# Performance work log

Measured on AMD Instinct MI355X. Metric: run time of the kernel, lower is better.

## Reference

```python
import jax, jax.numpy as jnp
import numpy as np

B, T, U, K, CDIM, S, M = 128, 600, 96, 10, 80, 512, 20
D1 = 3 + CDIM        # rnn1 input: x_t (3) + attention window w (CDIM)
D2 = 3 + S + CDIM    # rnn2 / rnn3 input: x_t + prev rnn out + w
OUT_DIM = 1 + 6 * M


def setup_inputs() -> dict:
    key = jax.random.key(0)
    ks = jax.random.split(key, 16)
    g = lambda k, shape: jax.random.normal(k, shape, jnp.float32) * 0.05
    z = lambda n: jnp.zeros((n,), jnp.float32)
    return {
        "x": jax.random.normal(ks[0], (B, T, 3), jnp.float32),
        "c_vec": jax.random.uniform(ks[1], (B, U, CDIM), jnp.float32),
        # FF cell 1 (input dim D1)
        "W_jx1": g(ks[2], (D1, S)), "b_jx1": z(S),
        "W_jh1": g(ks[3], (S, S)),  "b_jh1": z(S),
        "W_kx1": g(ks[4], (D1, S)), "b_kx1": z(S),
        "W_kh1": g(ks[5], (S, S)),  "b_kh1": z(S),
        # FF cell 2 (input dim D2) -- also used for the 3rd RNN (source reuses self.rnn2)
        "W_jx2": g(ks[6], (D2, S)), "b_jx2": z(S),
        "W_jh2": g(ks[7], (S, S)),  "b_jh2": z(S),
        "W_kx2": g(ks[8], (D2, S)), "b_kx2": z(S),
        "W_kh2": g(ks[9], (S, S)),  "b_kh2": z(S),
        # attention window head: S -> 3K
        "W_win": g(ks[10], (S, 3 * K)), "b_win": z(3 * K),
        # output head: S -> 1 + 6M
        "W_lin": g(ks[11], (S, OUT_DIM)), "b_lin": z(OUT_DIM),
    }


def _ff(inp, h, Wjx, bjx, Wjh, bjh, Wkx, bkx, Wkh, bkh):
    # custom gated cell: out = j*(1-h) + (1-k)*h
    j = jax.nn.sigmoid(inp @ Wjx + bjx + h @ Wjh + bjh)
    k = jax.nn.sigmoid(inp @ Wkx + bkx + h @ Wkh + bkh)
    return j * (1.0 - h) + (1.0 - k) * h


def reference(x, c_vec,
              W_jx1, b_jx1, W_jh1, b_jh1, W_kx1, b_kx1, W_kh1, b_kh1,
              W_jx2, b_jx2, W_jh2, b_jh2, W_kx2, b_kx2, W_kh2, b_kh2,
              W_win, b_win, W_lin, b_lin):
    u = jnp.arange(U, dtype=x.dtype)  # [U]

    def step(carry, xt):
        h1, h2, h3, kappa, w = carry  # h*: [B,S], kappa: [B,K], w: [B,CDIM]
        in1 = jnp.concatenate([xt, w], axis=-1)
        h1 = _ff(in1, h1, W_jx1, b_jx1, W_jh1, b_jh1, W_kx1, b_kx1, W_kh1, b_kh1)
        kg = h1 @ W_win + b_win                       # [B, 3K]
        a_hat, be_hat, k_hat = jnp.split(kg, 3, axis=1)
        alpha = jnp.exp(a_hat)                        # [B,K]
        beta = jnp.exp(be_hat)
        kappa = kappa + jnp.exp(k_hat)
        # phi[b,u] = sum_k alpha * exp(-beta * (kappa - u)^2)
        phi = jnp.sum(alpha[:, :, None] *
                      jnp.exp(-beta[:, :, None] * (kappa[:, :, None] - u) ** 2),
                      axis=1)                          # [B,U]
        w = jnp.einsum('bu,buc->bc', phi, c_vec)      # [B,CDIM]
        in2 = jnp.concatenate([xt, h1, w], axis=-1)
        h2 = _ff(in2, h2, W_jx2, b_jx2, W_jh2, b_jh2, W_kx2, b_kx2, W_kh2, b_kh2)
        in3 = jnp.concatenate([xt, h2, w], axis=-1)
        # source bug kept faithfully: third RNN reuses rnn2's weights
        h3 = _ff(in3, h3, W_jx2, b_jx2, W_jh2, b_jh2, W_kx2, b_kx2, W_kh2, b_kh2)
        return (h1, h2, h3, kappa, w), h3

    zS = jnp.zeros((B, S), x.dtype)
    init = (zS, zS, zS, jnp.zeros((B, K), x.dtype), jnp.zeros((B, CDIM), x.dtype))
    _, ys = jax.lax.scan(step, init, jnp.swapaxes(x, 0, 1))  # ys: [T,B,S]
    out_cat = jnp.swapaxes(ys, 0, 1).reshape(B * T, S)
    return out_cat @ W_lin + b_lin                    # [B*T, 1+6M]
```

## Files before the change

### kernel.cpp

```cpp
#include <hip/hip_runtime.h>
#include <hip/hip_bf16.h>

typedef __bf16 bf16;
typedef __bf16 bf16x8 __attribute__((ext_vector_type(8)));
typedef float  f32x4  __attribute__((ext_vector_type(4)));

#define AS1 __attribute__((address_space(1)))
#define AS3 __attribute__((address_space(3)))

#define NT   600
#define NB   128
#define NS   512
#define NU   96
#define NK   10
#define NC   80
#define NOUT 121

#define W1X_J 0
#define W1W_J 16384
#define W1H_J 65536
#define W1X_K 327680
#define W1W_K 344064
#define W1H_K 393216
#define W2X_J 655360
#define W2W_J 671744
#define W2A_J 720896
#define W2H_J 983040
#define W2X_K 1245184
#define W2W_K 1261568
#define W2A_K 1310720
#define W2H_K 1572864
#define WWIN  1835008
#define WLIN  1851392

#define BIAS_BYTE_OFF 3833856
#define H_BYTE_OFF    3842048
#define HBUF 65536
#define FLAG_BYTE_OFF 4659200
#define BAR_BYTE_OFF  4659264

#define HSTRIDE 520

#define AUX_SC0   1
#define AUX_SC0S1 17

__device__ __forceinline__ float ldIn(const void* q, long i, int isF32) {
  if (isF32) return ((const float*)q)[i];
  return (float)((const bf16*)q)[i];
}

struct KParams {
  const void* x;
  const void* c_vec;
  const void* b_win;
  const void* b_lin;
  const bf16* W;
  const float* bias;
  bf16* h1; bf16* h2; bf16* h3;
  void* out;
  const int* flag;
  int* bar;
};

template <int AUX>
__device__ __forceinline__ void stage_tile_async(const bf16* g, bf16* lds, int tid) {
  const int w = tid >> 6, lane = tid & 63;
#pragma unroll
  for (int r = 0; r < 4; ++r) {
    const int row = (w << 2) + r;
    __builtin_amdgcn_global_load_lds(
        (const AS1 void*)(g + (size_t)row * NS + (size_t)lane * 8),
        (AS3 void*)(lds + (size_t)row * HSTRIDE), 16, 0, AUX);
  }
}

__device__ __forceinline__ void group_arrive(int* gb) {
  __syncthreads();
  if (threadIdx.x == 0) {
    if ((__hip_atomic_fetch_add(gb, 1, __ATOMIC_RELAXED, __HIP_MEMORY_SCOPE_AGENT) & 31) == 31)
      __hip_atomic_fetch_add(gb + 8, 1, __ATOMIC_RELAXED, __HIP_MEMORY_SCOPE_AGENT);
  }
}
__device__ __forceinline__ void group_wait(int* gb, int target) {
  if (threadIdx.x == 0) {
    while (__hip_atomic_load(gb + 8, __ATOMIC_RELAXED, __HIP_MEMORY_SCOPE_AGENT) < target)
      __builtin_amdgcn_s_sleep(1);
  }
  __syncthreads();
  __atomic_signal_fence(__ATOMIC_ACQ_REL);
}

__device__ __forceinline__ void storeH(unsigned* dst, unsigned v, bool fast) {
  if (fast) *dst = v;
  else __hip_atomic_store(dst, v, __ATOMIC_RELAXED, __HIP_MEMORY_SCOPE_AGENT);
}

__global__ void sniff_kernel(const unsigned short* w, int* flag) {
  __shared__ int cnt;
  if (threadIdx.x == 0) cnt = 0;
  __syncthreads();
  int c = 0;
  for (int i = threadIdx.x; i < 8192; i += 256) {
    unsigned e = (w[2 * i] >> 7) & 0xFF;
    if (e == 0xFF || e < 96) c++;
  }
  atomicAdd(&cnt, c);
  __syncthreads();
  if (threadIdx.x == 0) *flag = (cnt > 512) ? 1 : 0;
}

__global__ void prep_kernel(const void* Wjx1, const void* Wjh1, const void* Wkx1, const void* Wkh1,
                            const void* Wjx2, const void* Wjh2, const void* Wkx2, const void* Wkh2,
                            const void* Wwin, const void* Wlin,
                            const void* bjx1, const void* bjh1, const void* bkx1, const void* bkh1,
                            const void* bjx2, const void* bjh2, const void* bkx2, const void* bkh2,
                            bf16* W, float* bias,
                            bf16* h1, bf16* h2, bf16* h3, int* bar,
                            const int* flag) {
  const int isF32 = *flag;
  const int r = blockIdx.y;
  const int e = blockIdx.x * 256 + threadIdx.x;
  if (r == 16) {
    if (e < 512) {
      bias[e]        = ldIn(bjx1, e, isF32) + ldIn(bjh1, e, isF32);
      bias[512 + e]  = ldIn(bkx1, e, isF32) + ldIn(bkh1, e, isF32);
      bias[1024 + e] = ldIn(bjx2, e, isF32) + ldIn(bjh2, e, isF32);
      bias[1536 + e] = ldIn(bkx2, e, isF32) + ldIn(bkh2, e, isF32);
    }
    return;
  }
  if (r == 17) {
    if (e < HBUF) {
      h1[HBUF + e] = (bf16)0.f;
      h2[HBUF + e] = (bf16)0.f;
      h3[HBUF + e] = (bf16)0.f;
    }
    if (e < 1024) bar[e] = 0;
    return;
  }
  const int   row0s[16]  = {0,3,0, 0,3,0, 0,515,3,0, 0,515,3,0, 0,0};
  const int   klens[16]  = {3,80,512, 3,80,512, 3,80,512,512, 3,80,512,512, 512,512};
  const int   kpads[16]  = {32,96,512, 32,96,512, 32,96,512,512, 32,96,512,512, 512,512};
  const int   cpads[16]  = {512,512,512, 512,512,512, 512,512,512,512, 512,512,512,512, 32,128};
  const int   nsrcs[16]  = {512,512,512, 512,512,512, 512,512,512,512, 512,512,512,512, 30,121};
  const long  offs[16]   = {W1X_J,W1W_J,W1H_J, W1X_K,W1W_K,W1H_K,
                            W2X_J,W2W_J,W2A_J,W2H_J, W2X_K,W2W_K,W2A_K,W2H_K, WWIN,WLIN};
  const void* srcs[16]   = {Wjx1,Wjx1,Wjh1, Wkx1,Wkx1,Wkh1,
                            Wjx2,Wjx2,Wjx2,Wjh2, Wkx2,Wkx2,Wkx2,Wkh2, Wwin,Wlin};
  const int Kpad = kpads[r], cp = cpads[r];
  const long tot = (long)Kpad * cp;
  if (e >= tot) return;
  const int j    = e & 7;
  const int lane = (e >> 3) & 63;
  const int rest = e >> 9;
  const int kbs  = Kpad >> 5;
  const int kb   = rest % kbs;
  const int slab = rest / kbs;
  const int col  = slab * 16 + (lane & 15);
  const int k    = kb * 32 + ((lane >> 4) << 3) + j;
  const int Klen = klens[r], row0 = row0s[r], N = nsrcs[r];
  bf16 v = (bf16)0.f;
  if (k < Klen && col < N) v = (bf16)ldIn(srcs[r], (long)(row0 + k) * N + col, isF32);
  W[offs[r] + e] = v;
}

__device__ __forceinline__ void accum_term(f32x4& acc, int& cnt, int kh,
    const bf16* Arow, int astride, const bf16* B, int kbs,
    int lr, int ko, int lane) {
  for (int kb = 0; kb < kbs; ++kb) {
    if (((cnt++) & 1) != kh) continue;
    bf16x8 a = *(const bf16x8*)(Arow + (size_t)lr * astride + kb * 32 + ko);
    bf16x8 b = *(const bf16x8*)(B + ((size_t)kb * 64 + lane) * 8);
    acc = __builtin_amdgcn_mfma_f32_16x16x32_bf16(a, b, acc, 0, 0, 0);
  }
}

__device__ __forceinline__ void accStore(float* d, const f32x4& a) {
  d[0] = a[0]; d[1] = a[1]; d[2] = a[2]; d[3] = a[3];
}

__global__ __launch_bounds__(256) void scan_kernel(KParams p) {
  const int isF32 = *p.flag;
  const int tid  = threadIdx.x;
  const int wid  = tid >> 6;
  const int lane = tid & 63;
  const int wg   = blockIdx.x;
  const int m    = wg & 7;
  const int slab = wg >> 3;
  const int m16  = m << 4;
  const int lr   = lane & 15;
  const int ko   = (lane >> 4) << 3;
  const int g    = wid >> 1;
  const int kh   = wid & 1;

  unsigned* hg1w = (unsigned*)p.h1;
  unsigned* hg2w = (unsigned*)p.h2;
  unsigned* hg3w = (unsigned*)p.h3;

  __shared__ alignas(16) bf16 wLds[32768];
  __shared__ alignas(16) bf16 h1L[16 * HSTRIDE];
  __shared__ alignas(16) bf16 h2L[16 * HSTRIDE];
  __shared__ alignas(16) bf16 h3L[16 * HSTRIDE];
  __shared__ alignas(16) bf16 xtL[16][32];
  __shared__ alignas(16) bf16 xt2L[16][32];
  __shared__ alignas(16) bf16 wL[16][96];
  __shared__ float kapL[16][NK];
  __shared__ float alphaL[16][NK];
  __shared__ float betaL[16][NK];
  __shared__ float phiL[16][NU];
  __shared__ float accA[4][64][5];
  __shared__ float accB[4][64][5];
  __shared__ bf16  hOutA[16][16];
  __shared__ bf16  hOutB[16][16];

  for (int i = tid; i < 16 * 32; i += 256) { (&xtL[0][0])[i] = (bf16)0.f; (&xt2L[0][0])[i] = (bf16)0.f; }
  for (int i = tid; i < 16 * 96; i += 256) (&wL[0][0])[i] = (bf16)0.f;
  for (int i = tid; i < 16 * NK; i += 256) (&kapL[0][0])[i] = 0.f;

  {
    const bf16* wsrc[4] = { p.W + W2A_J + (size_t)slab * (16 * NS),
                            p.W + W2A_K + (size_t)slab * (16 * NS),
                            p.W + W2H_J + (size_t)slab * (16 * NS),
                            p.W + W2H_K + (size_t)slab * (16 * NS) };
#pragma unroll
    for (int mt = 0; mt < 4; ++mt) {
#pragma unroll
      for (int r = 0; r < 4; ++r) {
        const int chunk = (wid << 2) + r;
        __builtin_amdgcn_global_load_lds(
            (const AS1 void*)(wsrc[mt] + chunk * 512 + lane * 8),
            (AS3 void*)(wLds + mt * 8192 + chunk * 512), 16, 0, 0);
      }
    }
  }
  __syncthreads();

  int* gb = p.bar + m * 64;
  {
    int xcc = __builtin_amdgcn_s_getreg((3 << 11) | (0 << 6) | 20) & 31;
    if (tid == 0) {
      __hip_atomic_fetch_or((unsigned*)(gb + 32), 1u << xcc,
                            __ATOMIC_RELAXED, __HIP_MEMORY_SCOPE_AGENT);
      __threadfence();
      if ((__hip_atomic_fetch_add(gb + 16, 1, __ATOMIC_RELAXED, __HIP_MEMORY_SCOPE_AGENT) & 31) == 31)
        __hip_atomic_fetch_add(gb + 24, 1, __ATOMIC_RELAXED, __HIP_MEMORY_SCOPE_AGENT);
      while (__hip_atomic_load(gb + 24, __ATOMIC_RELAXED, __HIP_MEMORY_SCOPE_AGENT) < 1)
        __builtin_amdgcn_s_sleep(1);
    }
    __syncthreads();
  }
  const unsigned msk = __hip_atomic_load((unsigned*)(gb + 32),
                                         __ATOMIC_RELAXED, __HIP_MEMORY_SCOPE_AGENT);
  const bool fast = (msk & (msk - 1)) == 0;

  int bt = 0;
  for (int t = -1; t < NT; ++t) {
    const int par_t = t & 1;
    const int par_p = (t + 1) & 1;

    if (t >= 0) {
      {
        const bf16* g1 = p.h1 + (size_t)par_t * HBUF + (size_t)m16 * NS;
        const bf16* g2 = p.h2 + (size_t)par_p * HBUF + (size_t)m16 * NS;
        const bf16* g3 = p.h3 + (size_t)par_p * HBUF + (size_t)m16 * NS;
        if (fast) {
          stage_tile_async<AUX_SC0>(g1, h1L, tid);
          stage_tile_async<AUX_SC0>(g2, h2L, tid);
          stage_tile_async<AUX_SC0>(g3, h3L, tid);
        } else {
          stage_tile_async<AUX_SC0S1>(g1, h1L, tid);
          stage_tile_async<AUX_SC0S1>(g2, h2L, tid);
          stage_tile_async<AUX_SC0S1>(g3, h3L, tid);
        }
      }
      __syncthreads();
      {
        int n2 = wid & 1, kh2 = wid >> 1;
        f32x4 acc = {0.f, 0.f, 0.f, 0.f};
        const bf16* B = p.W + WWIN + (size_t)n2 * (16 * NS);
        for (int kb = 0; kb < 16; ++kb) {
          if ((kb & 1) != kh2) continue;
          bf16x8 a = *(const bf16x8*)(h1L + (size_t)lr * HSTRIDE + kb * 32 + ko);
          bf16x8 b = *(const bf16x8*)(B + ((size_t)kb * 64 + lane) * 8);
          acc = __builtin_amdgcn_mfma_f32_16x16x32_bf16(a, b, acc, 0, 0, 0);
        }
        accStore(accA[wid][lane], acc);
      }
      __syncthreads();
      {
        int arow = tid >> 4, aj = tid & 15;
        float lo = 1e30f, hi = -1e30f;
        if (aj < NK) {
          const int rr = arow & 3;
          const int lbase = (arow >> 2) << 4;
          const int o0 = aj, o1 = NK + aj, o2 = 2 * NK + aj;
          float ah    = accA[o0 >> 4][lbase | (o0 & 15)][rr] + accA[(o0 >> 4) + 2][lbase | (o0 & 15)][rr]
                      + ldIn(p.b_win, o0, isF32);
          float bepre = accA[o1 >> 4][lbase | (o1 & 15)][rr] + accA[(o1 >> 4) + 2][lbase | (o1 & 15)][rr]
                      + ldIn(p.b_win, o1, isF32);
          float dkpre = accA[o2 >> 4][lbase | (o2 & 15)][rr] + accA[(o2 >> 4) + 2][lbase | (o2 & 15)][rr]
                      + ldIn(p.b_win, o2, isF32);
          float be = expf(bepre);
          float dk = expf(dkpre);
          float al = expf(ah);
          float kap = kapL[arow][aj] + dk;
          kapL[arow][aj] = kap;
          alphaL[arow][aj] = al;
          betaL[arow][aj] = be;
          float arg = (ah + 18.42f) / be;
          if (arg > 0.f) { float R = sqrtf(arg); lo = kap - R; hi = kap + R; }
        }
        lo = fminf(lo, __shfl_xor(lo, 1));  hi = fmaxf(hi, __shfl_xor(hi, 1));
        lo = fminf(lo, __shfl_xor(lo, 2));  hi = fmaxf(hi, __shfl_xor(hi, 2));
        lo = fminf(lo, __shfl_xor(lo, 4));  hi = fmaxf(hi, __shfl_xor(hi, 4));
        lo = fminf(lo, __shfl_xor(lo, 8));  hi = fmaxf(hi, __shfl_xor(hi, 8));
        const int ulo = (lo <= 0.f) ? 0 : ((lo > 95.f) ? 96 : (int)floorf(lo));
        const int uhi = (hi >= 95.f) ? 95 : ((hi < 0.f) ? -1 : (int)ceilf(hi));
        __syncthreads();
        for (int u = ulo + aj; u <= uhi; u += 16) {
          float s = 0.f, uf = (float)u;
          for (int k2 = 0; k2 < NK; ++k2) {
            float d = kapL[arow][k2] - uf;
            s += alphaL[arow][k2] * __expf(-betaL[arow][k2] * d * d);
          }
          phiL[arow][u] = s;
        }
        __syncthreads();
        if (isF32) {
          const float* cv = (const float*)p.c_vec + (long)(m16 + arow) * NU * NC;
          for (int ch = aj; ch < 20; ch += 16) {
            float a0 = 0.f, a1 = 0.f, a2 = 0.f, a3 = 0.f;
            for (int u = ulo; u <= uhi; ++u) {
              const float* q = cv + (long)u * NC + (ch << 2);
              float ph = phiL[arow][u];
              a0 += ph * q[0]; a1 += ph * q[1]; a2 += ph * q[2]; a3 += ph * q[3];
            }
            wL[arow][(ch << 2) + 0] = (bf16)a0;
            wL[arow][(ch << 2) + 1] = (bf16)a1;
            wL[arow][(ch << 2) + 2] = (bf16)a2;
            wL[arow][(ch << 2) + 3] = (bf16)a3;
          }
        } else {
          const long cv0 = (long)(m16 + arow) * NU * NC;
          for (int c = aj; c < NC; c += 16) {
            float acc = 0.f;
            for (int u = ulo; u <= uhi; ++u)
              acc += phiL[arow][u] * ldIn(p.c_vec, cv0 + (long)u * NC + c, isF32);
            wL[arow][c] = (bf16)acc;
          }
        }
      }
      __syncthreads();
      {
        f32x4 acc = {0.f, 0.f, 0.f, 0.f};
        int cnt = 0;
        const size_t oX = g ? W2X_K : W2X_J, oW = g ? W2W_K : W2W_J;
        const bf16* wA = wLds + (g ? 8192 : 0);
        const bf16* wH = wLds + (g ? 24576 : 16384);
        accum_term(acc, cnt, kh, &xtL[0][0], 32, p.W + oX + (size_t)slab * NS,        1,  lr, ko, lane);
        accum_term(acc, cnt, kh, h1L, HSTRIDE, wA, 16, lr, ko, lane);
        accum_term(acc, cnt, kh, &wL[0][0], 96, p.W + oW + (size_t)slab * (3 * NS),   3,  lr, ko, lane);
        accum_term(acc, cnt, kh, h2L, HSTRIDE, wH, 16, lr, ko, lane);
        accStore(accA[wid][lane], acc);
      }
      if (slab < 8 && t >= 1) {
        f32x4 acc = {0.f, 0.f, 0.f, 0.f};
        const bf16* B = p.W + WLIN + (size_t)slab * (16 * NS);
        for (int kb = 0; kb < 16; ++kb) {
          if ((kb & 3) != wid) continue;
          bf16x8 a = *(const bf16x8*)(h3L + (size_t)lr * HSTRIDE + kb * 32 + ko);
          bf16x8 b = *(const bf16x8*)(B + ((size_t)kb * 64 + lane) * 8);
          acc = __builtin_amdgcn_mfma_f32_16x16x32_bf16(a, b, acc, 0, 0, 0);
        }
        accStore(accB[wid][lane], acc);
      }
      __syncthreads();
      {
        int ls = tid & 63, r = tid >> 6;
        int s = (slab << 4) + (ls & 15);
        int rowIdx = ((ls >> 4) << 2) + r;
        float jp = accA[0][ls][r] + accA[1][ls][r] + p.bias[1024 + s];
        float kp = accA[2][ls][r] + accA[3][ls][r] + p.bias[1536 + s];
        float ho = (float)h2L[rowIdx * HSTRIDE + s];
        float jj = 1.f / (1.f + __expf(-jp));
        float kk = 1.f / (1.f + __expf(-kp));
        hOutA[rowIdx][ls & 15] = (bf16)(jj * (1.f - ho) + (1.f - kk) * ho);
      }
      if (slab < 8 && t >= 1 && tid < 64) {
        int o = (slab << 4) + (tid & 15);
        if (o < NOUT) {
          float bl = ldIn(p.b_lin, o, isF32);
          int rb = (tid >> 4) << 2;
          for (int r = 0; r < 4; ++r) {
            float v = accB[0][tid][r] + accB[1][tid][r] + accB[2][tid][r] + accB[3][tid][r] + bl;
            long oi = ((long)(m16 + rb + r) * NT + (t - 1)) * NOUT + o;
            if (isF32) ((float*)p.out)[oi] = v; else ((bf16*)p.out)[oi] = (bf16)v;
          }
        }
      }
      __syncthreads();
      if (tid < 128) {
        int row = tid >> 3, c = tid & 7;
        union { unsigned u; unsigned short s[2]; } v;
        union { bf16 b; unsigned short s; } a0, a1;
        a0.b = hOutA[row][2 * c]; a1.b = hOutA[row][2 * c + 1];
        v.s[0] = a0.s; v.s[1] = a1.s;
        storeH(hg2w + (size_t)par_t * (HBUF / 2) + (m16 + row) * 256 + slab * 8 + c, v.u, fast);
      }
      ++bt;
      group_arrive(gb);
      if (t < NT - 1) {
        f32x4 acc1 = {0.f, 0.f, 0.f, 0.f};
        int cnt = 0;
        const size_t oX = g ? W1X_K : W1X_J, oW = g ? W1W_K : W1W_J, oH = g ? W1H_K : W1H_J;
        accum_term(acc1, cnt, kh, &xt2L[0][0], 32, p.W + oX + (size_t)slab * NS,       1,  lr, ko, lane);
        accum_term(acc1, cnt, kh, &wL[0][0], 96, p.W + oW + (size_t)slab * (3 * NS),   3,  lr, ko, lane);
        accum_term(acc1, cnt, kh, h1L, HSTRIDE, p.W + oH + (size_t)slab * (16 * NS), 16, lr, ko, lane);
        accStore(accB[wid][lane], acc1);
      }
      group_wait(gb, bt);
    }

    if (t >= 0) {
      const bf16* g2 = p.h2 + (size_t)par_t * HBUF + (size_t)m16 * NS;
      if (fast) stage_tile_async<AUX_SC0>(g2, h2L, tid);
      else      stage_tile_async<AUX_SC0S1>(g2, h2L, tid);
    }
    if (t == -1) {
      const bf16* g1 = p.h1 + (size_t)HBUF + (size_t)m16 * NS;
      if (fast) stage_tile_async<AUX_SC0>(g1, h1L, tid);
      else      stage_tile_async<AUX_SC0S1>(g1, h1L, tid);
      if (tid < 48) {
        int row = tid / 3, d = tid - row * 3;
        xt2L[row][d] = (bf16)ldIn(p.x, ((long)(m16 + row) * NT + 0) * 3 + d, isF32);
      }
    }
    __syncthreads();
    f32x4 acc3 = {0.f, 0.f, 0.f, 0.f};
    if (t >= 0) {
      int cnt = 0;
      const size_t oX = g ? W2X_K : W2X_J, oW = g ? W2W_K : W2W_J;
      const bf16* wA = wLds + (g ? 8192 : 0);
      const bf16* wH = wLds + (g ? 24576 : 16384);
      accum_term(acc3, cnt, kh, &xtL[0][0], 32, p.W + oX + (size_t)slab * NS,        1,  lr, ko, lane);
      accum_term(acc3, cnt, kh, h2L, HSTRIDE, wA, 16, lr, ko, lane);
      accum_term(acc3, cnt, kh, &wL[0][0], 96, p.W + oW + (size_t)slab * (3 * NS),   3,  lr, ko, lane);
      accum_term(acc3, cnt, kh, h3L, HSTRIDE, wH, 16, lr, ko, lane);
    }
    accStore(accA[wid][lane], acc3);
    if (t == -1) {
      f32x4 acc1 = {0.f, 0.f, 0.f, 0.f};
      int cnt = 0;
      const size_t oX = g ? W1X_K : W1X_J, oW = g ? W1W_K : W1W_J, oH = g ? W1H_K : W1H_J;
      accum_term(acc1, cnt, kh, &xt2L[0][0], 32, p.W + oX + (size_t)slab * NS,       1,  lr, ko, lane);
      accum_term(acc1, cnt, kh, &wL[0][0], 96, p.W + oW + (size_t)slab * (3 * NS),   3,  lr, ko, lane);
      accum_term(acc1, cnt, kh, h1L, HSTRIDE, p.W + oH + (size_t)slab * (16 * NS), 16, lr, ko, lane);
      accStore(accB[wid][lane], acc1);
    }
    __syncthreads();
    {
      int ls = tid & 63, r = tid >> 6;
      int s = (slab << 4) + (ls & 15);
      int rowIdx = ((ls >> 4) << 2) + r;
      if (t >= 0) {
        float jp = accA[0][ls][r] + accA[1][ls][r] + p.bias[1024 + s];
        float kp = accA[2][ls][r] + accA[3][ls][r] + p.bias[1536 + s];
        float ho = (float)h3L[rowIdx * HSTRIDE + s];
        float jj = 1.f / (1.f + __expf(-jp));
        float kk = 1.f / (1.f + __expf(-kp));
        hOutA[rowIdx][ls & 15] = (bf16)(jj * (1.f - ho) + (1.f - kk) * ho);
      }
      if (t < NT - 1) {
        float jp = accB[0][ls][r] + accB[1][ls][r] + p.bias[0 + s];
        float kp = accB[2][ls][r] + accB[3][ls][r] + p.bias[512 + s];
        float ho = (float)h1L[rowIdx * HSTRIDE + s];
        float jj = 1.f / (1.f + __expf(-jp));
        float kk = 1.f / (1.f + __expf(-kp));
        hOutB[rowIdx][ls & 15] = (bf16)(jj * (1.f - ho) + (1.f - kk) * ho);
      }
    }
    __syncthreads();
    if (t >= 0 && tid < 128) {
      int row = tid >> 3, c = tid & 7;
      union { unsigned u; unsigned short s[2]; } v;
      union { bf16 b; unsigned short s; } a0, a1;
      a0.b = hOutA[row][2 * c]; a1.b = hOutA[row][2 * c + 1];
      v.s[0] = a0.s; v.s[1] = a1.s;
      storeH(hg3w + (size_t)par_t * (HBUF / 2) + (m16 + row) * 256 + slab * 8 + c, v.u, fast);
    }
    if (t < NT - 1 && tid >= 128) {
      int t2 = tid - 128;
      int row = t2 >> 3, c = t2 & 7;
      union { unsigned u; unsigned short s[2]; } v;
      union { bf16 b; unsigned short s; } a0, a1;
      a0.b = hOutB[row][2 * c]; a1.b = hOutB[row][2 * c + 1];
      v.s[0] = a0.s; v.s[1] = a1.s;
      storeH(hg1w + (size_t)par_p * (HBUF / 2) + (m16 + row) * 256 + slab * 8 + c, v.u, fast);
    }
    ++bt;
    group_arrive(gb);
    if (t + 1 < NT && tid < 48) {
      int row = tid / 3, d = tid - row * 3;
      xtL[row][d] = (bf16)ldIn(p.x, ((long)(m16 + row) * NT + (t + 1)) * 3 + d, isF32);
    }
    if (t + 2 < NT && tid >= 64 && tid < 112) {
      int t2 = tid - 64;
      int row = t2 / 3, d = t2 - row * 3;
      xt2L[row][d] = (bf16)ldIn(p.x, ((long)(m16 + row) * NT + (t + 2)) * 3 + d, isF32);
    }
    group_wait(gb, bt);
  }

  if (slab < 8) {
    const bf16* g3 = p.h3 + (size_t)HBUF + (size_t)m16 * NS;
    if (fast) stage_tile_async<AUX_SC0>(g3, h3L, tid);
    else      stage_tile_async<AUX_SC0S1>(g3, h3L, tid);
    __syncthreads();
    f32x4 acc = {0.f, 0.f, 0.f, 0.f};
    const bf16* B = p.W + WLIN + (size_t)slab * (16 * NS);
    for (int kb = 0; kb < 16; ++kb) {
      if ((kb & 3) != wid) continue;
      bf16x8 a = *(const bf16x8*)(h3L + (size_t)lr * HSTRIDE + kb * 32 + ko);
      bf16x8 b = *(const bf16x8*)(B + ((size_t)kb * 64 + lane) * 8);
      acc = __builtin_amdgcn_mfma_f32_16x16x32_bf16(a, b, acc, 0, 0, 0);
    }
    accStore(accB[wid][lane], acc);
    __syncthreads();
    if (tid < 64) {
      int o = (slab << 4) + (tid & 15);
      if (o < NOUT) {
        float bl = ldIn(p.b_lin, o, isF32);
        int rb = (tid >> 4) << 2;
        for (int r = 0; r < 4; ++r) {
          float v = accB[0][tid][r] + accB[1][tid][r] + accB[2][tid][r] + accB[3][tid][r] + bl;
          long oi = ((long)(m16 + rb + r) * NT + (NT - 1)) * NOUT + o;
          if (isF32) ((float*)p.out)[oi] = v; else ((bf16*)p.out)[oi] = (bf16)v;
        }
      }
    }
  }
}

extern "C" void kernel_launch(void* const* d_in, const int* in_sizes, int n_in,
                              void* d_out, int out_size, void* d_ws, size_t ws_size,
                              hipStream_t stream) {
  (void)in_sizes; (void)n_in; (void)out_size; (void)ws_size;

  bf16*  wsW  = (bf16*)d_ws;
  float* bias = (float*)((char*)d_ws + BIAS_BYTE_OFF);
  bf16*  h1   = (bf16*)((char*)d_ws + H_BYTE_OFF);
  bf16*  h2   = h1 + 2 * HBUF;
  bf16*  h3   = h2 + 2 * HBUF;
  int*   flag = (int*)((char*)d_ws + FLAG_BYTE_OFF);
  int*   bar  = (int*)((char*)d_ws + BAR_BYTE_OFF);

  sniff_kernel<<<1, 256, 0, stream>>>((const unsigned short*)d_in[4], flag);

  prep_kernel<<<dim3(1024, 18), 256, 0, stream>>>(
      d_in[2], d_in[4], d_in[6], d_in[8], d_in[10], d_in[12], d_in[14], d_in[16],
      d_in[18], d_in[20],
      d_in[3], d_in[5], d_in[7], d_in[9], d_in[11], d_in[13], d_in[15], d_in[17],
      wsW, bias, h1, h2, h3, bar, flag);

  KParams kp;
  kp.x = d_in[0]; kp.c_vec = d_in[1]; kp.b_win = d_in[19]; kp.b_lin = d_in[21];
  kp.W = wsW; kp.bias = bias;
  kp.h1 = h1; kp.h2 = h2; kp.h3 = h3;
  kp.out = d_out;
  kp.flag = flag;
  kp.bar = bar;

  scan_kernel<<<256, 256, 0, stream>>>(kp);
}
```

Measured before the change: 10.79 ms.

## Wavefront-pipeline the three RNN layers so each step needs one grid barrier

Restructures the time loop into a skewed software pipeline: iteration i computes layer1 at step i, layer2 at step i-1, layer3 at step i-2 and the output head at step i-3. The old loop used two group barriers per timestep. The new one uses a single barrier per iteration, and layer2's input-side partial sum is computed while waiting at that barrier. Ring buffers for x_t and the attention window, plus zero-initialised first h buffers, support the skew. The cost is more __syncthreads phases per iteration, two extra pipeline-fill iterations, and more LDS.

After: 10.44 ms. 1.03x faster.

```diff
diff --git a/kernel.cpp b/kernel.cpp
--- a/kernel.cpp
+++ b/kernel.cpp
@@ -131,9 +131,9 @@
   }
   if (r == 17) {
     if (e < HBUF) {
-      h1[HBUF + e] = (bf16)0.f;
-      h2[HBUF + e] = (bf16)0.f;
-      h3[HBUF + e] = (bf16)0.f;
+      h1[e] = (bf16)0.f; h1[HBUF + e] = (bf16)0.f;
+      h2[e] = (bf16)0.f; h2[HBUF + e] = (bf16)0.f;
+      h3[e] = (bf16)0.f; h3[HBUF + e] = (bf16)0.f;
     }
     if (e < 1024) bar[e] = 0;
     return;
@@ -201,21 +201,26 @@
   __shared__ alignas(16) bf16 h1L[16 * HSTRIDE];
   __shared__ alignas(16) bf16 h2L[16 * HSTRIDE];
   __shared__ alignas(16) bf16 h3L[16 * HSTRIDE];
-  __shared__ alignas(16) bf16 xtL[16][32];
-  __shared__ alignas(16) bf16 xt2L[16][32];
-  __shared__ alignas(16) bf16 wL[16][96];
+  __shared__ alignas(16) bf16 xtR[4][16][32];
+  __shared__ alignas(16) bf16 wR[3][16][96];
   __shared__ float kapL[16][NK];
   __shared__ float alphaL[16][NK];
   __shared__ float betaL[16][NK];
   __shared__ float phiL[16][NU];
   __shared__ float accA[4][64][5];
   __shared__ float accB[4][64][5];
-  __shared__ bf16  hOutA[16][16];
-  __shared__ bf16  hOutB[16][16];
-
-  for (int i = tid; i < 16 * 32; i += 256) { (&xtL[0][0])[i] = (bf16)0.f; (&xt2L[0][0])[i] = (bf16)0.f; }
-  for (int i = tid; i < 16 * 96; i += 256) (&wL[0][0])[i] = (bf16)0.f;
+  __shared__ bf16  hOut1[16][16];
+  __shared__ bf16  hOut2[16][16];
+  __shared__ bf16  hOut3[16][16];
+
+  for (int i = tid; i < 4 * 16 * 32; i += 256) (&xtR[0][0][0])[i] = (bf16)0.f;
+  for (int i = tid; i < 3 * 16 * 96; i += 256) (&wR[0][0][0])[i] = (bf16)0.f;
   for (int i = tid; i < 16 * NK; i += 256) (&kapL[0][0])[i] = 0.f;
+
+  const size_t oX2 = g ? W2X_K : W2X_J, oW2 = g ? W2W_K : W2W_J;
+  const size_t oX1 = g ? W1X_K : W1X_J, oW1 = g ? W1W_K : W1W_J, oH1 = g ? W1H_K : W1H_J;
+  const bf16* wA2 = wLds + (g ? 8192 : 0);
+  const bf16* wH2 = wLds + (g ? 24576 : 16384);
 
   {
     const bf16* wsrc[4] = { p.W + W2A_J + (size_t)slab * (16 * NS),
@@ -233,6 +238,10 @@
       }
     }
   }
+  if (tid < 48) {
+    int row = tid / 3, d = tid - row * 3;
+    xtR[0][row][d] = (bf16)ldIn(p.x, ((long)(m16 + row) * NT + 0) * 3 + d, isF32);
+  }
   __syncthreads();
 
   int* gb = p.bar + m * 64;
@@ -253,70 +262,198 @@
                                          __ATOMIC_RELAXED, __HIP_MEMORY_SCOPE_AGENT);
   const bool fast = (msk & (msk - 1)) == 0;
 
+  f32x4 acc2pre = {0.f, 0.f, 0.f, 0.f};
   int bt = 0;
-  for (int t = -1; t < NT; ++t) {
-    const int par_t = t & 1;
-    const int par_p = (t + 1) & 1;
-
-    if (t >= 0) {
-      {
-        const bf16* g1 = p.h1 + (size_t)par_t * HBUF + (size_t)m16 * NS;
-        const bf16* g2 = p.h2 + (size_t)par_p * HBUF + (size_t)m16 * NS;
-        const bf16* g3 = p.h3 + (size_t)par_p * HBUF + (size_t)m16 * NS;
-        if (fast) {
-          stage_tile_async<AUX_SC0>(g1, h1L, tid);
-          stage_tile_async<AUX_SC0>(g2, h2L, tid);
-          stage_tile_async<AUX_SC0>(g3, h3L, tid);
-        } else {
-          stage_tile_async<AUX_SC0S1>(g1, h1L, tid);
-          stage_tile_async<AUX_SC0S1>(g2, h2L, tid);
-          stage_tile_async<AUX_SC0S1>(g3, h3L, tid);
+
+  {
+    f32x4 acc = {0.f, 0.f, 0.f, 0.f};
+    int cnt = 0;
+    accum_term(acc, cnt, kh, &xtR[0][0][0], 32, p.W + oX1 + (size_t)slab * NS,       1, lr, ko, lane);
+    accum_term(acc, cnt, kh, &wR[0][0][0],  96, p.W + oW1 + (size_t)slab * (3 * NS), 3, lr, ko, lane);
+    accStore(accB[wid][lane], acc);
+    __syncthreads();
+    {
+      int ls = tid & 63, r = tid >> 6;
+      int s = (slab << 4) + (ls & 15);
+      int rowIdx = ((ls >> 4) << 2) + r;
+      float jp = accB[0][ls][r] + accB[1][ls][r] + p.bias[0 + s];
+      float jj = 1.f / (1.f + __expf(-jp));
+      hOut1[rowIdx][ls & 15] = (bf16)jj;
+    }
+    __syncthreads();
+    if (tid < 128) {
+      int row = tid >> 3, c = tid & 7;
+      union { unsigned u; unsigned short s[2]; } v;
+      union { bf16 b; unsigned short s; } a0, a1;
+      a0.b = hOut1[row][2 * c]; a1.b = hOut1[row][2 * c + 1];
+      v.s[0] = a0.s; v.s[1] = a1.s;
+      storeH(hg1w + (m16 + row) * 256 + slab * 8 + c, v.u, fast);
+    }
+    ++bt;
+    group_arrive(gb);
+    group_wait(gb, bt);
+  }
+
+  for (int i = 0; i <= NT + 2; ++i) {
+    const bool A1  = (i <= NT - 1);
+    const bool AF1 = (i <= NT - 2);
+    const bool A2  = (i >= 1 && i <= NT);
+    const bool A3  = (i >= 2 && i <= NT + 1);
+    const bool AO  = (i >= 3) && (slab < 8);
+    const bool APRE = (i <= NT - 1);
+
+    if (i >= 1 && i <= NT + 1) {
+      const bf16* g2 = p.h2 + (size_t)(i & 1) * HBUF + (size_t)m16 * NS;
+      if (fast) stage_tile_async<AUX_SC0>(g2, h2L, tid);
+      else      stage_tile_async<AUX_SC0S1>(g2, h2L, tid);
+    }
+    if (i >= 2) {
+      const bf16* g3 = p.h3 + (size_t)((i + 1) & 1) * HBUF + (size_t)m16 * NS;
+      if (fast) stage_tile_async<AUX_SC0>(g3, h3L, tid);
+      else      stage_tile_async<AUX_SC0S1>(g3, h3L, tid);
+    }
+    if (i <= NT - 2 && tid < 48) {
+      int row = tid / 3, d = tid - row * 3;
+      xtR[(i + 1) & 3][row][d] = (bf16)ldIn(p.x, ((long)(m16 + row) * NT + (i + 1)) * 3 + d, isF32);
+    }
+    __syncthreads();
+
+    if (A2) {
+      f32x4 acc = acc2pre;
+      int cnt = 20;
+      accum_term(acc, cnt, kh, h2L, HSTRIDE, wH2, 16, lr, ko, lane);
+      accStore(accA[wid][lane], acc);
+    }
+    if (AO) {
+      f32x4 acc = {0.f, 0.f, 0.f, 0.f};
+      const bf16* B = p.W + WLIN + (size_t)slab * (16 * NS);
+      for (int kb = 0; kb < 16; ++kb) {
+        if ((kb & 3) != wid) continue;
+        bf16x8 a = *(const bf16x8*)(h3L + (size_t)lr * HSTRIDE + kb * 32 + ko);
+        bf16x8 b = *(const bf16x8*)(B + ((size_t)kb * 64 + lane) * 8);
+        acc = __builtin_amdgcn_mfma_f32_16x16x32_bf16(a, b, acc, 0, 0, 0);
+      }
+      accStore(accB[wid][lane], acc);
+    }
+    __syncthreads();
+
+    if (A2) {
+      int ls = tid & 63, r = tid >> 6;
+      int s = (slab << 4) + (ls & 15);
+      int rowIdx = ((ls >> 4) << 2) + r;
+      float jp = accA[0][ls][r] + accA[1][ls][r] + p.bias[1024 + s];
+      float kp = accA[2][ls][r] + accA[3][ls][r] + p.bias[1536 + s];
+      float ho = (float)h2L[rowIdx * HSTRIDE + s];
+      float jj = 1.f / (1.f + __expf(-jp));
+      float kk = 1.f / (1.f + __expf(-kp));
+      hOut2[rowIdx][ls & 15] = (bf16)(jj * (1.f - ho) + (1.f - kk) * ho);
+    }
+    if (AO && tid < 64) {
+      int o = (slab << 4) + (tid & 15);
+      if (o < NOUT) {
+        float bl = ldIn(p.b_lin, o, isF32);
+        int rb = (tid >> 4) << 2;
+        for (int r = 0; r < 4; ++r) {
+          float v = accB[0][tid][r] + accB[1][tid][r] + accB[2][tid][r] + accB[3][tid][r] + bl;
+          long oi = ((long)(m16 + rb + r) * NT + (i - 3)) * NOUT + o;
+          if (isF32) ((float*)p.out)[oi] = v; else ((bf16*)p.out)[oi] = (bf16)v;
         }
       }
+    }
+    __syncthreads();
+
+    if (A3) {
+      f32x4 acc = {0.f, 0.f, 0.f, 0.f};
+      int cnt = 0;
+      accum_term(acc, cnt, kh, &xtR[(i - 2) & 3][0][0], 32, p.W + oX2 + (size_t)slab * NS,      1,  lr, ko, lane);
+      accum_term(acc, cnt, kh, h2L, HSTRIDE, wA2, 16, lr, ko, lane);
+      accum_term(acc, cnt, kh, &wR[(i - 2) % 3][0][0], 96, p.W + oW2 + (size_t)slab * (3 * NS), 3,  lr, ko, lane);
+      accum_term(acc, cnt, kh, h3L, HSTRIDE, wH2, 16, lr, ko, lane);
+      accStore(accA[wid][lane], acc);
+    }
+    if (A2 && tid < 128) {
+      int row = tid >> 3, c = tid & 7;
+      union { unsigned u; unsigned short s[2]; } v;
+      union { bf16 b; unsigned short s; } a0, a1;
+      a0.b = hOut2[row][2 * c]; a1.b = hOut2[row][2 * c + 1];
+      v.s[0] = a0.s; v.s[1] = a1.s;
+      storeH(hg2w + (size_t)((i - 1) & 1) * (HBUF / 2) + (m16 + row) * 256 + slab * 8 + c, v.u, fast);
+    }
+    __syncthreads();
+
+    if (A3) {
+      int ls = tid & 63, r = tid >> 6;
+      int s = (slab << 4) + (ls & 15);
+      int rowIdx = ((ls >> 4) << 2) + r;
+      float jp = accA[0][ls][r] + accA[1][ls][r] + p.bias[1024 + s];
+      float kp = accA[2][ls][r] + accA[3][ls][r] + p.bias[1536 + s];
+      float ho = (float)h3L[rowIdx * HSTRIDE + s];
+      float jj = 1.f / (1.f + __expf(-jp));
+      float kk = 1.f / (1.f + __expf(-kp));
+      hOut3[rowIdx][ls & 15] = (bf16)(jj * (1.f - ho) + (1.f - kk) * ho);
+    }
+    __syncthreads();
+
+    if (A1) {
+      const bf16* g1 = p.h1 + (size_t)(i & 1) * HBUF + (size_t)m16 * NS;
+      if (fast) stage_tile_async<AUX_SC0>(g1, h1L, tid);
+      else      stage_tile_async<AUX_SC0S1>(g1, h1L, tid);
+    }
+    if (A3 && tid < 128) {
+      int row = tid >> 3, c = tid & 7;
+      union { unsigned u; unsigned short s[2]; } v;
+      union { bf16 b; unsigned short s; } a0, a1;
+      a0.b = hOut3[row][2 * c]; a1.b = hOut3[row][2 * c + 1];
+      v.s[0] = a0.s; v.s[1] = a1.s;
+      storeH(hg3w + (size_t)((i - 2) & 1) * (HBUF / 2) + (m16 + row) * 256 + slab * 8 + c, v.u, fast);
+    }
+    __syncthreads();
+
+    if (A1) {
+      int n2 = wid & 1, kh2 = wid >> 1;
+      f32x4 acc = {0.f, 0.f, 0.f, 0.f};
+      const bf16* B = p.W + WWIN + (size_t)n2 * (16 * NS);
+      for (int kb = 0; kb < 16; ++kb) {
+        if ((kb & 1) != kh2) continue;
+        bf16x8 a = *(const bf16x8*)(h1L + (size_t)lr * HSTRIDE + kb * 32 + ko);
+        bf16x8 b = *(const bf16x8*)(B + ((size_t)kb * 64 + lane) * 8);
+        acc = __builtin_amdgcn_mfma_f32_16x16x32_bf16(a, b, acc, 0, 0, 0);
+      }
+      accStore(accA[wid][lane], acc);
+    }
+    __syncthreads();
+
+    {
+      int arow = tid >> 4, aj = tid & 15;
+      float lo = 1e30f, hi = -1e30f;
+      if (A1 && aj < NK) {
+        const int rr = arow & 3;
+        const int lbase = (arow >> 2) << 4;
+        const int o0 = aj, o1 = NK + aj, o2 = 2 * NK + aj;
+        float ah    = accA[o0 >> 4][lbase | (o0 & 15)][rr] + accA[(o0 >> 4) + 2][lbase | (o0 & 15)][rr]
+                    + ldIn(p.b_win, o0, isF32);
+        float bepre = accA[o1 >> 4][lbase | (o1 & 15)][rr] + accA[(o1 >> 4) + 2][lbase | (o1 & 15)][rr]
+                    + ldIn(p.b_win, o1, isF32);
+        float dkpre = accA[o2 >> 4][lbase | (o2 & 15)][rr] + accA[(o2 >> 4) + 2][lbase | (o2 & 15)][rr]
+                    + ldIn(p.b_win, o2, isF32);
+        float be = expf(bepre);
+        float dk = expf(dkpre);
+        float al = expf(ah);
+        float kap = kapL[arow][aj] + dk;
+        kapL[arow][aj] = kap;
+        alphaL[arow][aj] = al;
+        betaL[arow][aj] = be;
+        float arg = (ah + 18.42f) / be;
+        if (arg > 0.f) { float R = sqrtf(arg); lo = kap - R; hi = kap + R; }
+      }
+      lo = fminf(lo, __shfl_xor(lo, 1));  hi = fmaxf(hi, __shfl_xor(hi, 1));
+      lo = fminf(lo, __shfl_xor(lo, 2));  hi = fmaxf(hi, __shfl_xor(hi, 2));
+      lo = fminf(lo, __shfl_xor(lo, 4));  hi = fmaxf(hi, __shfl_xor(hi, 4));
+      lo = fminf(lo, __shfl_xor(lo, 8));  hi = fmaxf(hi, __shfl_xor(hi, 8));
+      const int ulo = (lo <= 0.f) ? 0 : ((lo > 95.f) ? 96 : (int)floorf(lo));
+      const int uhi = (hi >= 95.f) ? 95 : ((hi < 0.f) ? -1 : (int)ceilf(hi));
       __syncthreads();
-      {
-        int n2 = wid & 1, kh2 = wid >> 1;
-        f32x4 acc = {0.f, 0.f, 0.f, 0.f};
-        const bf16* B = p.W + WWIN + (size_t)n2 * (16 * NS);
-        for (int kb = 0; kb < 16; ++kb) {
-          if ((kb & 1) != kh2) continue;
-          bf16x8 a = *(const bf16x8*)(h1L + (size_t)lr * HSTRIDE + kb * 32 + ko);
-          bf16x8 b = *(const bf16x8*)(B + ((size_t)kb * 64 + lane) * 8);
-          acc = __builtin_amdgcn_mfma_f32_16x16x32_bf16(a, b, acc, 0, 0, 0);
-        }
-        accStore(accA[wid][lane], acc);
-      }
-      __syncthreads();
-      {
-        int arow = tid >> 4, aj = tid & 15;
-        float lo = 1e30f, hi = -1e30f;
-        if (aj < NK) {
-          const int rr = arow & 3;
-          const int lbase = (arow >> 2) << 4;
-          const int o0 = aj, o1 = NK + aj, o2 = 2 * NK + aj;
-          float ah    = accA[o0 >> 4][lbase | (o0 & 15)][rr] + accA[(o0 >> 4) + 2][lbase | (o0 & 15)][rr]
-                      + ldIn(p.b_win, o0, isF32);
-          float bepre = accA[o1 >> 4][lbase | (o1 & 15)][rr] + accA[(o1 >> 4) + 2][lbase | (o1 & 15)][rr]
-                      + ldIn(p.b_win, o1, isF32);
-          float dkpre = accA[o2 >> 4][lbase | (o2 & 15)][rr] + accA[(o2 >> 4) + 2][lbase | (o2 & 15)][rr]
-                      + ldIn(p.b_win, o2, isF32);
-          float be = expf(bepre);
-          float dk = expf(dkpre);
-          float al = expf(ah);
-          float kap = kapL[arow][aj] + dk;
-          kapL[arow][aj] = kap;
-          alphaL[arow][aj] = al;
-          betaL[arow][aj] = be;
-          float arg = (ah + 18.42f) / be;
-          if (arg > 0.f) { float R = sqrtf(arg); lo = kap - R; hi = kap + R; }
-        }
-        lo = fminf(lo, __shfl_xor(lo, 1));  hi = fmaxf(hi, __shfl_xor(hi, 1));
-        lo = fminf(lo, __shfl_xor(lo, 2));  hi = fmaxf(hi, __shfl_xor(hi, 2));
-        lo = fminf(lo, __shfl_xor(lo, 4));  hi = fmaxf(hi, __shfl_xor(hi, 4));
-        lo = fminf(lo, __shfl_xor(lo, 8));  hi = fmaxf(hi, __shfl_xor(hi, 8));
-        const int ulo = (lo <= 0.f) ? 0 : ((lo > 95.f) ? 96 : (int)floorf(lo));
-        const int uhi = (hi >= 95.f) ? 95 : ((hi < 0.f) ? -1 : (int)ceilf(hi));
-        __syncthreads();
+      if (A1) {
         for (int u = ulo + aj; u <= uhi; u += 16) {
           float s = 0.f, uf = (float)u;
           for (int k2 = 0; k2 < NK; ++k2) {
@@ -325,7 +462,10 @@
           }
           phiL[arow][u] = s;
         }
-        __syncthreads();
+      }
+      __syncthreads();
+      if (A1) {
+        bf16* wOut = &wR[i % 3][0][0];
         if (isF32) {
           const float* cv = (const float*)p.c_vec + (long)(m16 + arow) * NU * NC;
           for (int ch = aj; ch < 20; ch += 16) {
@@ -335,10 +475,10 @@
               float ph = phiL[arow][u];
               a0 += ph * q[0]; a1 += ph * q[1]; a2 += ph * q[2]; a3 += ph * q[3];
             }
-            wL[arow][(ch << 2) + 0] = (bf16)a0;
-            wL[arow][(ch << 2) + 1] = (bf16)a1;
-            wL[arow][(ch << 2) + 2] = (bf16)a2;
-            wL[arow][(ch << 2) + 3] = (bf16)a3;
+            wOut[arow * 96 + (ch << 2) + 0] = (bf16)a0;
+            wOut[arow * 96 + (ch << 2) + 1] = (bf16)a1;
+            wOut[arow * 96 + (ch << 2) + 2] = (bf16)a2;
+            wOut[arow * 96 + (ch << 2) + 3] = (bf16)a3;
           }
         } else {
           const long cv0 = (long)(m16 + arow) * NU * NC;
@@ -346,197 +486,56 @@
             float acc = 0.f;
             for (int u = ulo; u <= uhi; ++u)
               acc += phiL[arow][u] * ldIn(p.c_vec, cv0 + (long)u * NC + c, isF32);
-            wL[arow][c] = (bf16)acc;
+            wOut[arow * 96 + c] = (bf16)acc;
           }
         }
       }
-      __syncthreads();
-      {
-        f32x4 acc = {0.f, 0.f, 0.f, 0.f};
-        int cnt = 0;
-        const size_t oX = g ? W2X_K : W2X_J, oW = g ? W2W_K : W2W_J;
-        const bf16* wA = wLds + (g ? 8192 : 0);
-        const bf16* wH = wLds + (g ? 24576 : 16384);
-        accum_term(acc, cnt, kh, &xtL[0][0], 32, p.W + oX + (size_t)slab * NS,        1,  lr, ko, lane);
-        accum_term(acc, cnt, kh, h1L, HSTRIDE, wA, 16, lr, ko, lane);
-        accum_term(acc, cnt, kh, &wL[0][0], 96, p.W + oW + (size_t)slab * (3 * NS),   3,  lr, ko, lane);
-        accum_term(acc, cnt, kh, h2L, HSTRIDE, wH, 16, lr, ko, lane);
-        accStore(accA[wid][lane], acc);
-      }
-      if (slab < 8 && t >= 1) {
-        f32x4 acc = {0.f, 0.f, 0.f, 0.f};
-        const bf16* B = p.W + WLIN + (size_t)slab * (16 * NS);
-        for (int kb = 0; kb < 16; ++kb) {
-          if ((kb & 3) != wid) continue;
-          bf16x8 a = *(const bf16x8*)(h3L + (size_t)lr * HSTRIDE + kb * 32 + ko);
-          bf16x8 b = *(const bf16x8*)(B + ((size_t)kb * 64 + lane) * 8);
-          acc = __builtin_amdgcn_mfma_f32_16x16x32_bf16(a, b, acc, 0, 0, 0);
-        }
-        accStore(accB[wid][lane], acc);
-      }
-      __syncthreads();
-      {
-        int ls = tid & 63, r = tid >> 6;
-        int s = (slab << 4) + (ls & 15);
-        int rowIdx = ((ls >> 4) << 2) + r;
-        float jp = accA[0][ls][r] + accA[1][ls][r] + p.bias[1024 + s];
-        float kp = accA[2][ls][r] + accA[3][ls][r] + p.bias[1536 + s];
-        float ho = (float)h2L[rowIdx * HSTRIDE + s];
-        float jj = 1.f / (1.f + __expf(-jp));
-        float kk = 1.f / (1.f + __expf(-kp));
-        hOutA[rowIdx][ls & 15] = (bf16)(jj * (1.f - ho) + (1.f - kk) * ho);
-      }
-      if (slab < 8 && t >= 1 && tid < 64) {
-        int o = (slab << 4) + (tid & 15);
-        if (o < NOUT) {
-          float bl = ldIn(p.b_lin, o, isF32);
-          int rb = (tid >> 4) << 2;
-          for (int r = 0; r < 4; ++r) {
-            float v = accB[0][tid][r] + accB[1][tid][r] + accB[2][tid][r] + accB[3][tid][r] + bl;
-            long oi = ((long)(m16 + rb + r) * NT + (t - 1)) * NOUT + o;
-            if (isF32) ((float*)p.out)[oi] = v; else ((bf16*)p.out)[oi] = (bf16)v;
-          }
-        }
-      }
-      __syncthreads();
-      if (tid < 128) {
-        int row = tid >> 3, c = tid & 7;
-        union { unsigned u; unsigned short s[2]; } v;
-        union { bf16 b; unsigned short s; } a0, a1;
-        a0.b = hOutA[row][2 * c]; a1.b = hOutA[row][2 * c + 1];
-        v.s[0] = a0.s; v.s[1] = a1.s;
-        storeH(hg2w + (size_t)par_t * (HBUF / 2) + (m16 + row) * 256 + slab * 8 + c, v.u, fast);
-      }
-      ++bt;
-      group_arrive(gb);
-      if (t < NT - 1) {
-        f32x4 acc1 = {0.f, 0.f, 0.f, 0.f};
-        int cnt = 0;
-        const size_t oX = g ? W1X_K : W1X_J, oW = g ? W1W_K : W1W_J, oH = g ? W1H_K : W1H_J;
-        accum_term(acc1, cnt, kh, &xt2L[0][0], 32, p.W + oX + (size_t)slab * NS,       1,  lr, ko, lane);
-        accum_term(acc1, cnt, kh, &wL[0][0], 96, p.W + oW + (size_t)slab * (3 * NS),   3,  lr, ko, lane);
-        accum_term(acc1, cnt, kh, h1L, HSTRIDE, p.W + oH + (size_t)slab * (16 * NS), 16, lr, ko, lane);
-        accStore(accB[wid][lane], acc1);
-      }
-      group_wait(gb, bt);
-    }
-
-    if (t >= 0) {
-      const bf16* g2 = p.h2 + (size_t)par_t * HBUF + (size_t)m16 * NS;
-      if (fast) stage_tile_async<AUX_SC0>(g2, h2L, tid);
-      else      stage_tile_async<AUX_SC0S1>(g2, h2L, tid);
-    }
-    if (t == -1) {
-      const bf16* g1 = p.h1 + (size_t)HBUF + (size_t)m16 * NS;
-      if (fast) stage_tile_async<AUX_SC0>(g1, h1L, tid);
-      else      stage_tile_async<AUX_SC0S1>(g1, h1L, tid);
-      if (tid < 48) {
-        int row = tid / 3, d = tid - row * 3;
-        xt2L[row][d] = (bf16)ldIn(p.x, ((long)(m16 + row) * NT + 0) * 3 + d, isF32);
-      }
-    }
-    __syncthreads();
-    f32x4 acc3 = {0.f, 0.f, 0.f, 0.f};
-    if (t >= 0) {
+    }
+    __syncthreads();
+
+    if (AF1) {
+      f32x4 acc = {0.f, 0.f, 0.f, 0.f};
       int cnt = 0;
-      const size_t oX = g ? W2X_K : W2X_J, oW = g ? W2W_K : W2W_J;
-      const bf16* wA = wLds + (g ? 8192 : 0);
-      const bf16* wH = wLds + (g ? 24576 : 16384);
-      accum_term(acc3, cnt, kh, &xtL[0][0], 32, p.W + oX + (size_t)slab * NS,        1,  lr, ko, lane);
-      accum_term(acc3, cnt, kh, h2L, HSTRIDE, wA, 16, lr, ko, lane);
-      accum_term(acc3, cnt, kh, &wL[0][0], 96, p.W + oW + (size_t)slab * (3 * NS),   3,  lr, ko, lane);
-      accum_term(acc3, cnt, kh, h3L, HSTRIDE, wH, 16, lr, ko, lane);
-    }
-    accStore(accA[wid][lane], acc3);
-    if (t == -1) {
-      f32x4 acc1 = {0.f, 0.f, 0.f, 0.f};
-      int cnt = 0;
-      const size_t oX = g ? W1X_K : W1X_J, oW = g ? W1W_K : W1W_J, oH = g ? W1H_K : W1H_J;
-      accum_term(acc1, cnt, kh, &xt2L[0][0], 32, p.W + oX + (size_t)slab * NS,       1,  lr, ko, lane);
-      accum_term(acc1, cnt, kh, &wL[0][0], 96, p.W + oW + (size_t)slab * (3 * NS),   3,  lr, ko, lane);
-      accum_term(acc1, cnt, kh, h1L, HSTRIDE, p.W + oH + (size_t)slab * (16 * NS), 16, lr, ko, lane);
-      accStore(accB[wid][lane], acc1);
-    }
-    __syncthreads();
-    {
+      accum_term(acc, cnt, kh, &xtR[(i + 1) & 3][0][0], 32, p.W + oX1 + (size_t)slab * NS,      1,  lr, ko, lane);
+      accum_term(acc, cnt, kh, &wR[i % 3][0][0], 96, p.W + oW1 + (size_t)slab * (3 * NS),       3,  lr, ko, lane);
+      accum_term(acc, cnt, kh, h1L, HSTRIDE, p.W + oH1 + (size_t)slab * (16 * NS), 16, lr, ko, lane);
+      accStore(accB[wid][lane], acc);
+    }
+    __syncthreads();
+
+    if (AF1) {
       int ls = tid & 63, r = tid >> 6;
       int s = (slab << 4) + (ls & 15);
       int rowIdx = ((ls >> 4) << 2) + r;
-      if (t >= 0) {
-        float jp = accA[0][ls][r] + accA[1][ls][r] + p.bias[1024 + s];
-        float kp = accA[2][ls][r] + accA[3][ls][r] + p.bias[1536 + s];
-        float ho = (float)h3L[rowIdx * HSTRIDE + s];
-        float jj = 1.f / (1.f + __expf(-jp));
-        float kk = 1.f / (1.f + __expf(-kp));
-        hOutA[rowIdx][ls & 15] = (bf16)(jj * (1.f - ho) + (1.f - kk) * ho);
-      }
-      if (t < NT - 1) {
-        float jp = accB[0][ls][r] + accB[1][ls][r] + p.bias[0 + s];
-        float kp = accB[2][ls][r] + accB[3][ls][r] + p.bias[512 + s];
-        float ho = (float)h1L[rowIdx * HSTRIDE + s];
-        float jj = 1.f / (1.f + __expf(-jp));
-        float kk = 1.f / (1.f + __expf(-kp));
-        hOutB[rowIdx][ls & 15] = (bf16)(jj * (1.f - ho) + (1.f - kk) * ho);
-      }
-    }
-    __syncthreads();
-    if (t >= 0 && tid < 128) {
+      float jp = accB[0][ls][r] + accB[1][ls][r] + p.bias[0 + s];
+      float kp = accB[2][ls][r] + accB[3][ls][r] + p.bias[512 + s];
+      float ho = (float)h1L[rowIdx * HSTRIDE + s];
+      float jj = 1.f / (1.f + __expf(-jp));
+      float kk = 1.f / (1.f + __expf(-kp));
+      hOut1[rowIdx][ls & 15] = (bf16)(jj * (1.f - ho) + (1.f - kk) * ho);
+    }
+    __syncthreads();
+    if (AF1 && tid < 128) {
       int row = tid >> 3, c = tid & 7;
       union { unsigned u; unsigned short s[2]; } v;
       union { bf16 b; unsigned short s; } a0, a1;
-      a0.b = hOutA[row][2 * c]; a1.b = hOutA[row][2 * c + 1];
+      a0.b = hOut1[row][2 * c]; a1.b = hOut1[row][2 * c + 1];
       v.s[0] = a0.s; v.s[1] = a1.s;
-      storeH(hg3w + (size_t)par_t * (HBUF / 2) + (m16 + row) * 256 + slab * 8 + c, v.u, fast);
-    }
-    if (t < NT - 1 && tid >= 128) {
-      int t2 = tid - 128;
-      int row = t2 >> 3, c = t2 & 7;
-      union { unsigned u; unsigned short s[2]; } v;
-      union { bf16 b; unsigned short s; } a0, a1;
-      a0.b = hOutB[row][2 * c]; a1.b = hOutB[row][2 * c + 1];
-      v.s[0] = a0.s; v.s[1] = a1.s;
-      storeH(hg1w + (size_t)par_p * (HBUF / 2) + (m16 + row) * 256 + slab * 8 + c, v.u, fast);
-    }
-    ++bt;
-    group_arrive(gb);
-    if (t + 1 < NT && tid < 48) {
-      int row = tid / 3, d = tid - row * 3;
-      xtL[row][d] = (bf16)ldIn(p.x, ((long)(m16 + row) * NT + (t + 1)) * 3 + d, isF32);
-    }
-    if (t + 2 < NT && tid >= 64 && tid < 112) {
-      int t2 = tid - 64;
-      int row = t2 / 3, d = t2 - row * 3;
-      xt2L[row][d] = (bf16)ldIn(p.x, ((long)(m16 + row) * NT + (t + 2)) * 3 + d, isF32);
-    }
-    group_wait(gb, bt);
-  }
-
-  if (slab < 8) {
-    const bf16* g3 = p.h3 + (size_t)HBUF + (size_t)m16 * NS;
-    if (fast) stage_tile_async<AUX_SC0>(g3, h3L, tid);
-    else      stage_tile_async<AUX_SC0S1>(g3, h3L, tid);
-    __syncthreads();
-    f32x4 acc = {0.f, 0.f, 0.f, 0.f};
-    const bf16* B = p.W + WLIN + (size_t)slab * (16 * NS);
-    for (int kb = 0; kb < 16; ++kb) {
-      if ((kb & 3) != wid) continue;
-      bf16x8 a = *(const bf16x8*)(h3L + (size_t)lr * HSTRIDE + kb * 32 + ko);
-      bf16x8 b = *(const bf16x8*)(B + ((size_t)kb * 64 + lane) * 8);
-      acc = __builtin_amdgcn_mfma_f32_16x16x32_bf16(a, b, acc, 0, 0, 0);
-    }
-    accStore(accB[wid][lane], acc);
-    __syncthreads();
-    if (tid < 64) {
-      int o = (slab << 4) + (tid & 15);
-      if (o < NOUT) {
-        float bl = ldIn(p.b_lin, o, isF32);
-        int rb = (tid >> 4) << 2;
-        for (int r = 0; r < 4; ++r) {
-          float v = accB[0][tid][r] + accB[1][tid][r] + accB[2][tid][r] + accB[3][tid][r] + bl;
-          long oi = ((long)(m16 + rb + r) * NT + (NT - 1)) * NOUT + o;
-          if (isF32) ((float*)p.out)[oi] = v; else ((bf16*)p.out)[oi] = (bf16)v;
-        }
-      }
+      storeH(hg1w + (size_t)((i + 1) & 1) * (HBUF / 2) + (m16 + row) * 256 + slab * 8 + c, v.u, fast);
+    }
+
+    if (i < NT + 2) {
+      ++bt;
+      group_arrive(gb);
+      if (APRE) {
+        f32x4 a = {0.f, 0.f, 0.f, 0.f};
+        int cnt = 0;
+        accum_term(a, cnt, kh, &xtR[i & 3][0][0], 32, p.W + oX2 + (size_t)slab * NS,      1,  lr, ko, lane);
+        accum_term(a, cnt, kh, h1L, HSTRIDE, wA2, 16, lr, ko, lane);
+        accum_term(a, cnt, kh, &wR[i % 3][0][0], 96, p.W + oW2 + (size_t)slab * (3 * NS), 3,  lr, ko, lane);
+        acc2pre = a;
+      }
+      group_wait(gb, bt);
     }
   }
 }
```
